# Kernel optimization log

Measured on AMD Instinct MI355X. Metric: run time of the kernel, lower is better.

## Reference

```python
import jax, jax.numpy as jnp
import numpy as np
from jax import lax

K = 5      # reassembly kernel
D = 2      # delta (downsample factor)


def _conv(x, w, b, stride=1, pad=0):
    y = lax.conv_general_dilated(x, w, (stride, stride), [(pad, pad), (pad, pad)],
                                 dimension_numbers=("NCHW", "OIHW", "NCHW"))
    return y + b[None, :, None, None]


def setup_inputs() -> dict:
    key = jax.random.key(0)
    ks = jax.random.split(key, 7)
    inC, outC, Cm = 64, 64, 64
    N, H, W = 2, 256, 256
    return {
        "x": jax.random.normal(ks[0], (N, inC, H, W), jnp.float32),
        "down_w": jax.random.normal(ks[1], (Cm, inC, 1, 1), jnp.float32) * 0.1,
        "down_b": jax.random.normal(ks[2], (Cm,), jnp.float32) * 0.1,
        "enc_w": jax.random.normal(ks[3], (K * K, Cm, 3, 3), jnp.float32) * 0.1,
        "enc_b": jax.random.normal(ks[4], (K * K,), jnp.float32) * 0.1,
        "out_w": jax.random.normal(ks[5], (outC, inC * D * D, 1, 1), jnp.float32) * 0.1,
        "out_b": jax.random.normal(ks[6], (outC,), jnp.float32) * 0.1,
    }


def reference(x, down_w, down_b, enc_w, enc_b, out_w, out_b):
    N, C, H, W = x.shape
    Hd, Wd = H // D, W // D
    p = K // 2

    # kernel prediction branch
    k = _conv(x, down_w, down_b)                       # (N, Cm, H, W)
    k = _conv(k, enc_w, enc_b, stride=D, pad=1)        # (N, K*K, Hd, Wd)
    k = jax.nn.softmax(k, axis=1)
    k = k.transpose(0, 2, 3, 1)                        # (N, Hd, Wd, K*K)

    # overlapping K x K windows at every (h, w): (N, C, H, W, K*K)
    xp = jnp.pad(x, ((0, 0), (0, 0), (p, p), (p, p)))
    patches = jnp.stack([xp[:, :, i:i + H, j:j + W]
                         for i in range(K) for j in range(K)], axis=-1)
    # faithful torch reshape (row-major reinterpretation, NOT space-to-depth)
    patches = patches.reshape(N, C * D * D, Hd, Wd, K * K)
    patches = patches.transpose(0, 2, 3, 1, 4)         # (N, Hd, Wd, C*D*D, K*K)

    out = jnp.einsum("nhwck,nhwk->nhwc", patches, k)   # weighted reassembly
    out = out.transpose(0, 3, 1, 2)                    # (N, C*D*D, Hd, Wd)
    return _conv(out, out_w, out_b)
```

## Files before the change

kernel.cpp:

```cpp
#include <hip/hip_runtime.h>
#include <hip/hip_bf16.h>

using u16 = unsigned short;
typedef __attribute__((ext_vector_type(8))) short bf16x8;
typedef __attribute__((ext_vector_type(4))) float f32x4;

static constexpr int N  = 2;
static constexpr int C  = 64;
static constexpr int H  = 256;
static constexpr int W  = 256;
static constexpr int Hd = 128;
static constexpr int Wd = 128;
static constexpr int KK = 25;
static constexpr int C2 = 256;
static constexpr int OC = 64;
static constexpr int HWP  = H * W;
static constexpr int HDWD = Hd * Wd;

__device__ __forceinline__ float bflo(unsigned u) { return __uint_as_float(u << 16); }
__device__ __forceinline__ float bfhi(unsigned u) { return __uint_as_float(u & 0xffff0000u); }
__device__ __forceinline__ unsigned pack2(float a, float b) {
    __hip_bfloat16 ha = __float2bfloat16(a), hb = __float2bfloat16(b);
    union { __hip_bfloat16 h; u16 u; } ua{ha}, ub{hb};
    return (unsigned)ua.u | ((unsigned)ub.u << 16);
}
__device__ __forceinline__ u16 f2bf(float f) {
    union { __hip_bfloat16 h; u16 u; } v{__float2bfloat16(f)};
    return v.u;
}

__global__ __launch_bounds__(256) void kA_down(const float* __restrict__ x,
                                               const float* __restrict__ w,
                                               const float* __restrict__ b,
                                               u16* __restrict__ k1) {
    __shared__ u16   xt[64][128];
    __shared__ float wt[64][66];
    const int tid = threadIdx.x;
    const int pg0 = blockIdx.x * 128;
    const int n   = pg0 >> 16;
    const int px0 = pg0 & (HWP - 1);

#pragma unroll
    for (int i = 0; i < 16; ++i) {
        int e  = i * 256 + tid;
        int cm = e >> 6, c = e & 63;
        wt[c][cm] = w[e];
    }
    const float* xb = x + (size_t)n * C * HWP + px0;
#pragma unroll
    for (int i = 0; i < 8; ++i) {
        int flat = i * 256 + tid;
        int row  = flat >> 5;
        int col4 = flat & 31;
        float4 v = *(const float4*)(xb + (size_t)row * HWP + col4 * 4);
        uint2 p;
        p.x = pack2(v.x, v.y);
        p.y = pack2(v.z, v.w);
        *(uint2*)&xt[row][col4 * 4] = p;
    }
    __syncthreads();

    const int cg  = tid & 7;
    const int pxg = tid >> 3;
    float acc[8][4];
#pragma unroll
    for (int j = 0; j < 8; ++j) {
        float bj = b[cg * 8 + j];
#pragma unroll
        for (int p = 0; p < 4; ++p) acc[j][p] = bj;
    }
#pragma unroll 8
    for (int c = 0; c < 64; ++c) {
        uint2 xv = *(const uint2*)&xt[c][pxg * 4];
        float xs[4] = {bflo(xv.x), bfhi(xv.x), bflo(xv.y), bfhi(xv.y)};
        float2 w01 = *(const float2*)&wt[c][cg * 8 + 0];
        float2 w23 = *(const float2*)&wt[c][cg * 8 + 2];
        float2 w45 = *(const float2*)&wt[c][cg * 8 + 4];
        float2 w67 = *(const float2*)&wt[c][cg * 8 + 6];
        float wv[8] = {w01.x, w01.y, w23.x, w23.y, w45.x, w45.y, w67.x, w67.y};
#pragma unroll
        for (int j = 0; j < 8; ++j)
#pragma unroll
            for (int p = 0; p < 4; ++p) acc[j][p] = fmaf(wv[j], xs[p], acc[j][p]);
    }
#pragma unroll
    for (int p = 0; p < 4; ++p) {
        uint4 o;
        o.x = pack2(acc[0][p], acc[1][p]);
        o.y = pack2(acc[2][p], acc[3][p]);
        o.z = pack2(acc[4][p], acc[5][p]);
        o.w = pack2(acc[6][p], acc[7][p]);
        *(uint4*)(k1 + ((size_t)pg0 + pxg * 4 + p) * 64 + cg * 8) = o;
    }
}

__global__ __launch_bounds__(256) void kW_pack(const float* __restrict__ ew,
                                               const float* __restrict__ ow,
                                               u16* __restrict__ bfr,
                                               u16* __restrict__ bfr2) {
    int idx = blockIdx.x * 256 + threadIdx.x;
    if (idx < 2304) {
        int l  = idx & 63;
        int ft = idx >> 6;
        int t  = ft & 1, s = ft >> 1;
        int tap = s >> 1, h = s & 1;
        int c = l & 15, q = l >> 4;
        int kk = t * 16 + c;
        u16 o[8];
#pragma unroll
        for (int j = 0; j < 8; ++j) {
            int cm = 32 * h + 8 * q + j;
            float v = (kk < 25) ? ew[(kk * 64 + cm) * 9 + tap] : 0.f;
            o[j] = f2bf(v);
        }
        *(uint4*)(bfr + (size_t)idx * 8) = *(uint4*)o;
    } else if (idx < 4352) {
        int i2 = idx - 2304;
        int l  = i2 & 63;
        int ft = i2 >> 6;
        int nt = ft & 3, s = ft >> 2;
        int c = l & 15, q = l >> 4;
        int co = nt * 16 + c;
        u16 o[8];
#pragma unroll
        for (int j = 0; j < 8; ++j)
            o[j] = f2bf(ow[co * 256 + s * 32 + q * 8 + j]);
        *(uint4*)(bfr2 + (size_t)i2 * 8) = *(uint4*)o;
    }
}

__global__ __launch_bounds__(256) void kB2_enc(const u16* __restrict__ k1,
                                               const u16* __restrict__ bfr,
                                               const float* __restrict__ eb,
                                               float* __restrict__ ksm) {
    __shared__ u16 tile[3 * 130 * 72];
    const int tid = threadIdx.x;
    const int b   = blockIdx.x;
    const int half = b & 1;
    const int hd   = (b >> 1) & 127;
    const int n    = b >> 8;
    const int w0 = half * 64;
    const int xb = 2 * w0 - 1;
    const int y0 = 2 * hd - 1;
    const u16* kb = k1 + (size_t)n * HWP * 64;

    for (int r = 0; r < 13; ++r) {
        int f = r * 256 + tid;
        if (f < 3096) {
            int p  = f >> 3, ch = f & 7;
            int y  = p / 129, xi = p - y * 129;
            int yy = y0 + y, xx = xb + xi;
            uint4 v = make_uint4(0u, 0u, 0u, 0u);
            if (yy >= 0 && xx >= 0 && xx < 256)
                v = *(const uint4*)(kb + ((size_t)(yy * W + xx)) * 64 + ch * 8);
            *(uint4*)&tile[(y * 130 + xi) * 72 + ch * 8] = v;
        }
    }
    __syncthreads();

    const int wv = tid >> 6;
    const int l  = tid & 63;
    const int c  = l & 15;
    const int q  = l >> 4;

    f32x4 acc0 = {0.f, 0.f, 0.f, 0.f};
    f32x4 acc1 = {0.f, 0.f, 0.f, 0.f};
#pragma unroll
    for (int s = 0; s < 18; ++s) {
        const int tap = s >> 1, h = s & 1;
        const int dy = tap / 3, dx = tap - dy * 3;
        const u16* ap = &tile[(dy * 130 + 32 * wv + 2 * c + dx) * 72 + 32 * h + 8 * q];
        bf16x8 a  = *(const bf16x8*)ap;
        bf16x8 b0 = *(const bf16x8*)(bfr + ((size_t)(s * 2 + 0) * 64 + l) * 8);
        bf16x8 b1 = *(const bf16x8*)(bfr + ((size_t)(s * 2 + 1) * 64 + l) * 8);
        acc0 = __builtin_amdgcn_mfma_f32_16x16x32_bf16(a, b0, acc0, 0, 0, 0);
        acc1 = __builtin_amdgcn_mfma_f32_16x16x32_bf16(a, b1, acc1, 0, 0, 0);
    }

    const float e0 = eb[c];
    const float e1 = eb[min(16 + c, 24)];
    const bool c9 = (c < 9);

#pragma unroll
    for (int r = 0; r < 4; ++r) {
        float l0 = acc0[r] + e0;
        float l1 = c9 ? (acc1[r] + e1) : -1e30f;
        float mx = fmaxf(l0, l1);
#pragma unroll
        for (int d = 1; d < 16; d <<= 1) mx = fmaxf(mx, __shfl_xor(mx, d, 64));
        float x0 = __expf(l0 - mx);
        float x1 = c9 ? __expf(l1 - mx) : 0.f;
        float sm = x0 + x1;
#pragma unroll
        for (int d = 1; d < 16; d <<= 1) sm += __shfl_xor(sm, d, 64);
        float inv = 1.f / sm;
        int wd = w0 + 16 * wv + q * 4 + r;
        float* op = ksm + (size_t)n * KK * HDWD + hd * Wd + wd;
        op[(size_t)c * HDWD] = x0 * inv;
        if (c9) op[(size_t)(16 + c) * HDWD] = x1 * inv;
    }
}

__global__ __launch_bounds__(256) void kC4_reassemble(const float* __restrict__ x,
                                                      const float* __restrict__ ksm,
                                                      u16* __restrict__ out2p) {
    __shared__ float xts[4 * 6 * 272];
    __shared__ u16   obuf[512][24];
    const int tid = threadIdx.x;
    const int b   = blockIdx.x;
    const int cc  = b & 15;
    const int hdt = (b >> 4) & 31;
    const int n   = b >> 9;
    const int hd0 = hdt * 4;
    const int hdo = tid >> 6;
    const int wdg = tid & 63;
    const int hd  = hd0 + hdo;
    const int wd0 = wdg * 2;
    const int w0  = ((hdo & 1) << 7) + wd0;
    const int lr0 = hdo >> 1;
    const int c0  = cc * 4;
    const int p0  = hdo * 128 + wd0;

    const float* kb = ksm + (size_t)n * KK * HDWD + hd * Wd + wd0;
    float2 kw[25];
#pragma unroll
    for (int kk = 0; kk < 25; ++kk) kw[kk] = *(const float2*)(kb + (size_t)kk * HDWD);

    int  soff[7];
    bool sval[7];
#pragma unroll
    for (int k = 0; k < 7; ++k) {
        int s = tid + 256 * k;
        int strip = s / 408;
        int rem   = s - 408 * strip;
        int r     = rem / 68;
        int c4    = rem - 68 * r;
        int y     = strip * 64 + (hd0 >> 1) - 2 + r;
        sval[k] = (s < 1632) & (c4 >= 1) & (c4 <= 64) & (y >= 0) & (y < H);
        int yc  = min(max(y, 0), H - 1);
        soff[k] = yc * W + (c4 - 1) * 4;
    }

    const float4 z = make_float4(0.f, 0.f, 0.f, 0.f);

#pragma unroll 1
    for (int ci = 0; ci < 4; ++ci) {
        __syncthreads();
        const float* base = x + (size_t)(n * C + c0 + ci) * HWP;
#pragma unroll
        for (int k = 0; k < 7; ++k) {
            int s = tid + 256 * k;
            if (s < 1632) {
                float4 v = sval[k] ? *(const float4*)(base + soff[k]) : z;
                *(float4*)&xts[4 * s] = v;
            }
        }
        __syncthreads();

        float a0[4], a1[4];
#pragma unroll
        for (int q = 0; q < 4; ++q) {
            float s0 = 0.f, s1 = 0.f;
#pragma unroll
            for (int i = 0; i < 5; ++i) {
                const float* rr = &xts[(q * 6 + lr0 + i) * 272 + w0 + 2];
                float2 r0 = *(const float2*)(rr + 0);
                float2 r1 = *(const float2*)(rr + 2);
                float2 r2 = *(const float2*)(rr + 4);
                float f[6] = {r0.x, r0.y, r1.x, r1.y, r2.x, r2.y};
#pragma unroll
                for (int j = 0; j < 5; ++j) {
                    const float2 kv = kw[i * 5 + j];
                    s0 = fmaf(f[j + 0], kv.x, s0);
                    s1 = fmaf(f[j + 1], kv.y, s1);
                }
            }
            a0[q] = s0; a1[q] = s1;
        }
        *(uint2*)&obuf[p0][ci * 4]     = make_uint2(pack2(a0[0], a0[1]), pack2(a0[2], a0[3]));
        *(uint2*)&obuf[p0 + 1][ci * 4] = make_uint2(pack2(a1[0], a1[1]), pack2(a1[2], a1[3]));
    }
    __syncthreads();

    u16* dst = out2p + ((size_t)(n * HDWD + hd * Wd + wd0)) * 256 + cc * 16;
    uint4 wa = *(const uint4*)&obuf[p0][0];
    uint4 wb = *(const uint4*)&obuf[p0][8];
    *(uint4*)(dst + 0) = wa;
    *(uint4*)(dst + 8) = wb;
    uint4 wc = *(const uint4*)&obuf[p0 + 1][0];
    uint4 wd_ = *(const uint4*)&obuf[p0 + 1][8];
    *(uint4*)(dst + 256 + 0) = wc;
    *(uint4*)(dst + 256 + 8) = wd_;
}

__global__ __launch_bounds__(256) void kD2_out(const u16* __restrict__ out2p,
                                               const u16* __restrict__ bfr2,
                                               const float* __restrict__ ob,
                                               float* __restrict__ out) {
    const int tid = threadIdx.x;
    const int b   = blockIdx.x;
    const int px0g = b * 64;
    const int n    = px0g >> 14;
    const int px0  = px0g & (HDWD - 1);
    const int nt = tid >> 6;
    const int l  = tid & 63;
    const int c  = l & 15;
    const int q  = l >> 4;

    const u16* A = out2p + (size_t)px0g * 256;

    f32x4 acc[4] = {{0.f,0.f,0.f,0.f},{0.f,0.f,0.f,0.f},
                    {0.f,0.f,0.f,0.f},{0.f,0.f,0.f,0.f}};
#pragma unroll
    for (int s = 0; s < 8; ++s) {
        bf16x8 bf = *(const bf16x8*)(bfr2 + ((size_t)(s * 4 + nt) * 64 + l) * 8);
#pragma unroll
        for (int mt = 0; mt < 4; ++mt) {
            const u16* ap = A + ((size_t)(mt * 16 + c)) * 256 + s * 32 + q * 8;
            bf16x8 a = *(const bf16x8*)ap;
            acc[mt] = __builtin_amdgcn_mfma_f32_16x16x32_bf16(a, bf, acc[mt], 0, 0, 0);
        }
    }
    const int co = nt * 16 + c;
    const float bias = ob[co];
    float* ob_ = out + (size_t)(n * OC + co) * HDWD + px0;
#pragma unroll
    for (int mt = 0; mt < 4; ++mt)
#pragma unroll
        for (int r = 0; r < 4; ++r)
            ob_[mt * 16 + q * 4 + r] = acc[mt][r] + bias;
}

extern "C" void kernel_launch(void* const* d_in, const int* in_sizes, int n_in,
                              void* d_out, int out_size, void* d_ws, size_t ws_size,
                              hipStream_t stream) {
    const float* x  = (const float*)d_in[0];
    const float* dw = (const float*)d_in[1];
    const float* db = (const float*)d_in[2];
    const float* ew = (const float*)d_in[3];
    const float* eb = (const float*)d_in[4];
    const float* ow = (const float*)d_in[5];
    const float* ob = (const float*)d_in[6];
    float* out = (float*)d_out;

    char* ws = (char*)d_ws;
    u16*   k1    = (u16*)ws;
    float* ksm   = (float*)(ws + 16777216);
    u16*   out2p = (u16*)(ws + 16777216 + 3276800);
    u16*   bfr   = out2p;
    u16*   bfr2  = (u16*)(ws + 16777216 + 3276800 + 16777216);

    kW_pack <<<dim3(18),   dim3(256), 0, stream>>>(ew, ow, bfr, bfr2);
    kA_down <<<dim3(1024), dim3(256), 0, stream>>>(x, dw, db, k1);
    kB2_enc <<<dim3(512),  dim3(256), 0, stream>>>(k1, bfr, eb, ksm);
    kC4_reassemble<<<dim3(1024), dim3(256), 0, stream>>>(x, ksm, out2p);
    kD2_out <<<dim3(512),  dim3(256), 0, stream>>>(out2p, bfr2, ob, out);
}
```

Baseline: 160.3 us.

## Widen reassembly tiles to four outputs per thread and drop LDS output staging

The reassembly kernel now gives each block 8 downsampled rows, and each thread computes 4 adjacent output pixels instead of 2. This halves the grid and raises reuse of the loaded x rows and softmax weights. The shared-memory output buffer is removed: packed bf16 results stay in registers and go straight to global memory, which drops one barrier and the LDS round trip. Padding columns are zeroed once and tile loads are simplified. The cost is more registers (100 weight floats plus accumulators) under a 2-blocks-per-SM launch bound, which risks spilling or lower occupancy.

Result: slower. 191.9 us (+19.8%).

```diff
diff --git a/kernel.cpp b/kernel.cpp
--- a/kernel.cpp
+++ b/kernel.cpp
@@ -201,96 +201,106 @@
     }
 }
 
-__global__ __launch_bounds__(256) void kC4_reassemble(const float* __restrict__ x,
-                                                      const float* __restrict__ ksm,
-                                                      u16* __restrict__ out2p) {
-    __shared__ float xts[4 * 6 * 272];
-    __shared__ u16   obuf[512][24];
+__global__ __launch_bounds__(256, 2) void kC5_reassemble(const float* __restrict__ x,
+                                                         const float* __restrict__ ksm,
+                                                         u16* __restrict__ out2p) {
+    __shared__ float xts[4 * 8 * 272];
     const int tid = threadIdx.x;
     const int b   = blockIdx.x;
     const int cc  = b & 15;
-    const int hdt = (b >> 4) & 31;
-    const int n   = b >> 9;
-    const int hd0 = hdt * 4;
-    const int hdo = tid >> 6;
-    const int wdg = tid & 63;
+    const int hdt = (b >> 4) & 15;
+    const int n   = b >> 8;
+    const int hd0 = hdt * 8;
+    const int t0  = hdt * 4;
+    const int hdo = tid >> 5;
+    const int wdg = tid & 31;
     const int hd  = hd0 + hdo;
-    const int wd0 = wdg * 2;
-    const int w0  = ((hdo & 1) << 7) + wd0;
-    const int lr0 = hdo >> 1;
+    const int wd0 = wdg * 4;
+    const int wb  = ((hdo & 1) << 7) + wd0;
+    const int rloc = hdo >> 1;
     const int c0  = cc * 4;
-    const int p0  = hdo * 128 + wd0;
+
+    if (tid < 64) {
+        int rr = tid >> 1, side = tid & 1;
+        int col = side ? 258 : 0;
+        *(float2*)&xts[rr * 272 + col] = make_float2(0.f, 0.f);
+    }
 
     const float* kb = ksm + (size_t)n * KK * HDWD + hd * Wd + wd0;
-    float2 kw[25];
-#pragma unroll
-    for (int kk = 0; kk < 25; ++kk) kw[kk] = *(const float2*)(kb + (size_t)kk * HDWD);
-
-    int  soff[7];
-    bool sval[7];
-#pragma unroll
-    for (int k = 0; k < 7; ++k) {
-        int s = tid + 256 * k;
-        int strip = s / 408;
-        int rem   = s - 408 * strip;
-        int r     = rem / 68;
-        int c4    = rem - 68 * r;
-        int y     = strip * 64 + (hd0 >> 1) - 2 + r;
-        sval[k] = (s < 1632) & (c4 >= 1) & (c4 <= 64) & (y >= 0) & (y < H);
-        int yc  = min(max(y, 0), H - 1);
-        soff[k] = yc * W + (c4 - 1) * 4;
-    }
-
-    const float4 z = make_float4(0.f, 0.f, 0.f, 0.f);
-
-#pragma unroll 1
+    float4 kwv[25];
+#pragma unroll
+    for (int t = 0; t < 25; ++t) kwv[t] = *(const float4*)(kb + (size_t)t * HDWD);
+
+    int  soff[8];
+    bool sval[8];
+#pragma unroll
+    for (int k = 0; k < 8; ++k) {
+        int s     = k * 256 + tid;
+        int c4    = s & 63;
+        int row   = (s >> 6) & 7;
+        int strip = s >> 9;
+        int y     = strip * 64 + t0 - 2 + row;
+        sval[k]   = (y >= 0) & (y < H);
+        int yc    = min(max(y, 0), H - 1);
+        soff[k]   = yc * W + c4 * 4;
+    }
+
+    unsigned outw[4][8];
+    const float4 z4 = make_float4(0.f, 0.f, 0.f, 0.f);
+
+#pragma unroll
     for (int ci = 0; ci < 4; ++ci) {
         __syncthreads();
         const float* base = x + (size_t)(n * C + c0 + ci) * HWP;
 #pragma unroll
-        for (int k = 0; k < 7; ++k) {
-            int s = tid + 256 * k;
-            if (s < 1632) {
-                float4 v = sval[k] ? *(const float4*)(base + soff[k]) : z;
-                *(float4*)&xts[4 * s] = v;
-            }
+        for (int k = 0; k < 8; ++k) {
+            int s = k * 256 + tid;
+            float4 v = sval[k] ? *(const float4*)(base + soff[k]) : z4;
+            int widx = (s >> 6) * 272 + 2 + (s & 63) * 4;
+            *(float2*)&xts[widx]     = make_float2(v.x, v.y);
+            *(float2*)&xts[widx + 2] = make_float2(v.z, v.w);
         }
         __syncthreads();
 
-        float a0[4], a1[4];
+        float sq[4][4];
+#pragma unroll
+        for (int q = 0; q < 4; ++q)
+#pragma unroll
+            for (int r = 0; r < 4; ++r) sq[q][r] = 0.f;
+
 #pragma unroll
         for (int q = 0; q < 4; ++q) {
-            float s0 = 0.f, s1 = 0.f;
 #pragma unroll
             for (int i = 0; i < 5; ++i) {
-                const float* rr = &xts[(q * 6 + lr0 + i) * 272 + w0 + 2];
-                float2 r0 = *(const float2*)(rr + 0);
-                float2 r1 = *(const float2*)(rr + 2);
-                float2 r2 = *(const float2*)(rr + 4);
-                float f[6] = {r0.x, r0.y, r1.x, r1.y, r2.x, r2.y};
+                const float* rp = &xts[(q * 8 + rloc + i) * 272 + wb];
+                float4 fa = *(const float4*)(rp);
+                float4 fb = *(const float4*)(rp + 4);
+                float f[8] = {fa.x, fa.y, fa.z, fa.w, fb.x, fb.y, fb.z, fb.w};
 #pragma unroll
                 for (int j = 0; j < 5; ++j) {
-                    const float2 kv = kw[i * 5 + j];
-                    s0 = fmaf(f[j + 0], kv.x, s0);
-                    s1 = fmaf(f[j + 1], kv.y, s1);
+                    const float4 kv = kwv[i * 5 + j];
+                    sq[q][0] = fmaf(f[j + 0], kv.x, sq[q][0]);
+                    sq[q][1] = fmaf(f[j + 1], kv.y, sq[q][1]);
+                    sq[q][2] = fmaf(f[j + 2], kv.z, sq[q][2]);
+                    sq[q][3] = fmaf(f[j + 3], kv.w, sq[q][3]);
                 }
             }
-            a0[q] = s0; a1[q] = s1;
-        }
-        *(uint2*)&obuf[p0][ci * 4]     = make_uint2(pack2(a0[0], a0[1]), pack2(a0[2], a0[3]));
-        *(uint2*)&obuf[p0 + 1][ci * 4] = make_uint2(pack2(a1[0], a1[1]), pack2(a1[2], a1[3]));
-    }
-    __syncthreads();
+        }
+#pragma unroll
+        for (int r = 0; r < 4; ++r) {
+            outw[r][ci * 2 + 0] = pack2(sq[0][r], sq[1][r]);
+            outw[r][ci * 2 + 1] = pack2(sq[2][r], sq[3][r]);
+        }
+    }
 
     u16* dst = out2p + ((size_t)(n * HDWD + hd * Wd + wd0)) * 256 + cc * 16;
-    uint4 wa = *(const uint4*)&obuf[p0][0];
-    uint4 wb = *(const uint4*)&obuf[p0][8];
-    *(uint4*)(dst + 0) = wa;
-    *(uint4*)(dst + 8) = wb;
-    uint4 wc = *(const uint4*)&obuf[p0 + 1][0];
-    uint4 wd_ = *(const uint4*)&obuf[p0 + 1][8];
-    *(uint4*)(dst + 256 + 0) = wc;
-    *(uint4*)(dst + 256 + 8) = wd_;
+#pragma unroll
+    for (int r = 0; r < 4; ++r) {
+        uint4 wa  = make_uint4(outw[r][0], outw[r][1], outw[r][2], outw[r][3]);
+        uint4 wb2 = make_uint4(outw[r][4], outw[r][5], outw[r][6], outw[r][7]);
+        *(uint4*)(dst + (size_t)r * 256 + 0) = wa;
+        *(uint4*)(dst + (size_t)r * 256 + 8) = wb2;
+    }
 }
 
 __global__ __launch_bounds__(256) void kD2_out(const u16* __restrict__ out2p,
@@ -353,6 +363,6 @@
     kW_pack <<<dim3(18),   dim3(256), 0, stream>>>(ew, ow, bfr, bfr2);
     kA_down <<<dim3(1024), dim3(256), 0, stream>>>(x, dw, db, k1);
     kB2_enc <<<dim3(512),  dim3(256), 0, stream>>>(k1, bfr, eb, ksm);
-    kC4_reassemble<<<dim3(1024), dim3(256), 0, stream>>>(x, ksm, out2p);
+    kC5_reassemble<<<dim3(512), dim3(256), 0, stream>>>(x, ksm, out2p);
     kD2_out <<<dim3(512),  dim3(256), 0, stream>>>(out2p, bfr2, ob, out);
 }
```
